# Kernel optimization log

Measured on AMD Instinct MI355X. Metric: run time of the kernel, lower is better.

The kernel has to match this reference:

```python
import jax, jax.numpy as jnp
import numpy as np

B, CIN, COUT, H, W = 8, 64, 64, 56, 56
HEAD, KATT, KCONV = 1, 5, 3
HEAD_DIM = COUT // HEAD
PAD = (1 * (KATT - 1) + 1) // 2  # dilation=1 -> 2


def setup_inputs() -> dict:
    key = jax.random.key(0)
    ks = jax.random.split(key, 12)
    n = jax.random.normal
    return {
        'x': n(ks[0], (B, CIN, H, W), jnp.float32),
        'w1': n(ks[1], (COUT, CIN), jnp.float32) * 0.05,
        'b1': n(ks[2], (COUT,), jnp.float32) * 0.05,
        'w2': n(ks[3], (COUT, CIN), jnp.float32) * 0.05,
        'b2': n(ks[4], (COUT,), jnp.float32) * 0.05,
        'w3': n(ks[5], (COUT, CIN), jnp.float32) * 0.05,
        'b3': n(ks[6], (COUT,), jnp.float32) * 0.05,
        'wp': n(ks[7], (HEAD_DIM, 2), jnp.float32) * 0.05,
        'bp': n(ks[8], (HEAD_DIM,), jnp.float32) * 0.05,
        'w_fc': n(ks[9], (KCONV * KCONV, 3 * HEAD), jnp.float32) * 0.05,
        'w_dep': n(ks[10], (COUT, KCONV * KCONV, KCONV, KCONV), jnp.float32) * 0.05,
        'b_dep': n(ks[11], (COUT,), jnp.float32) * 0.05,
        'rate1': jnp.full((1,), 0.5, jnp.float32),
        'rate2': jnp.full((1,), 0.5, jnp.float32),
    }


def _conv1x1(x, w, b):
    return jnp.einsum('oc,bchw->bohw', w, x) + b[None, :, None, None]


def _unfold(x, h, w):
    # reflection-pad then extract KATTxKATT patches -> (n, c, KATT*KATT, h, w)
    p = jnp.pad(x, ((0, 0), (0, 0), (PAD, PAD), (PAD, PAD)), mode='reflect')
    return jnp.stack([p[:, :, i:i + h, j:j + w]
                      for i in range(KATT) for j in range(KATT)], axis=2)


def reference(x, w1, b1, w2, b2, w3, b3, wp, bp, w_fc, w_dep, b_dep, rate1, rate2):
    b, _, h, w = x.shape
    q = _conv1x1(x, w1, b1)
    k = _conv1x1(x, w2, b2)
    v = _conv1x1(x, w3, b3)
    head_dim = wp.shape[0]
    head = q.shape[1] // head_dim
    scaling = float(head_dim) ** -0.5

    # relative position embedding (stride=1 so q_pe == pe)
    loc_w = jnp.tile(jnp.linspace(-1.0, 1.0, w)[None, :], (h, 1))
    loc_h = jnp.tile(jnp.linspace(-1.0, 1.0, h)[:, None], (1, w))
    pe = _conv1x1(jnp.stack([loc_w, loc_h])[None], wp, bp)  # (1, head_dim, h, w)

    q_att = q.reshape(b * head, head_dim, h, w) * scaling
    k_att = k.reshape(b * head, head_dim, h, w)
    v_att = v.reshape(b * head, head_dim, h, w)

    unfold_k = _unfold(k_att, h, w)          # (b*head, d, 25, h, w)
    unfold_rpe = _unfold(pe, h, w)           # (1, d, 25, h, w)
    att = jnp.sum(q_att[:, :, None] * (unfold_k + pe[:, :, None] - unfold_rpe), axis=1)
    att = jax.nn.softmax(att, axis=1)        # softmax over the 25 window positions
    unfold_v = _unfold(v_att, h, w)
    out_att = jnp.sum(att[:, None] * unfold_v, axis=2).reshape(b, -1, h, w)

    # parallel depthwise-conv branch
    f_cat = jnp.concatenate([q.reshape(b, head, head_dim, h * w),
                             k.reshape(b, head, head_dim, h * w),
                             v.reshape(b, head, head_dim, h * w)], axis=1)  # (b, 3h, d, hw)
    f_all = jnp.einsum('oc,bcdl->bodl', w_fc, f_cat)                        # (b, 9, d, hw)
    f_conv = jnp.transpose(f_all, (0, 2, 1, 3)).reshape(b, head_dim * KCONV * KCONV, h, w)
    out_conv = jax.lax.conv_general_dilated(
        f_conv, w_dep, window_strides=(1, 1), padding=((1, 1), (1, 1)),
        feature_group_count=head_dim,
        dimension_numbers=('NCHW', 'OIHW', 'NCHW')) + b_dep[None, :, None, None]

    return rate1[0] * out_att + rate2[0] * out_conv
```

## Files before the change

kernel.cpp:

```cpp
#include <hip/hip_runtime.h>

#define HH 56
#define WWID 56
#define HWP (HH*WWID)
#define BB 8
#define CC 64
#define NPIX (BB*HWP)

__device__ __forceinline__ float grp_sum(float x) {
  int xi;
  xi = __builtin_amdgcn_update_dpp(0, __float_as_int(x), 0xB1, 0xF, 0xF, true);
  x += __int_as_float(xi);
  xi = __builtin_amdgcn_update_dpp(0, __float_as_int(x), 0x4E, 0xF, 0xF, true);
  x += __int_as_float(xi);
  xi = __builtin_amdgcn_update_dpp(0, __float_as_int(x), 0x141, 0xF, 0xF, true);
  x += __int_as_float(xi);
  xi = __builtin_amdgcn_update_dpp(0, __float_as_int(x), 0x140, 0xF, 0xF, true);
  x += __int_as_float(xi);
  return x;
}

__device__ __forceinline__ float dot4(float4 a, float4 b) {
  float t = a.x * b.x;
  t = fmaf(a.y, b.y, t);
  t = fmaf(a.z, b.z, t);
  t = fmaf(a.w, b.w, t);
  return t;
}

__global__ __launch_bounds__(256) void prep_kernel(
    const float* __restrict__ w1, const float* __restrict__ w2, const float* __restrict__ w3,
    const float* __restrict__ w_fc, const float* __restrict__ w_dep,
    float* __restrict__ w1P, float* __restrict__ w2P, float* __restrict__ w3P,
    float* __restrict__ tab)
{
  const int t = threadIdx.x;
  for (int idx = t; idx < 64*64; idx += 256) {
    int c4 = idx >> 8, r = idx & 255, o = r >> 2, e = r & 3;
    int c = c4*4 + e;
    w1P[idx] = w1[o*64 + c];
    w2P[idx] = w2[o*64 + c];
    w3P[idx] = w3[o*64 + c];
  }
  for (int idx = t; idx < 27*64; idx += 256) {
    int d = idx & 63, bt = idx >> 6;
    int br = bt / 9, tap = bt - br*9;
    float s = 0.f;
    #pragma unroll
    for (int oo = 0; oo < 9; ++oo)
      s += w_dep[d*81 + oo*9 + tap] * w_fc[oo*3 + br];
    tab[idx] = s;
  }
}

__global__ __launch_bounds__(256) void qkv_kernel(
    const float* __restrict__ x,
    const float* __restrict__ b1, const float* __restrict__ b2, const float* __restrict__ b3,
    const float* __restrict__ w1P, const float* __restrict__ w2P, const float* __restrict__ w3P,
    float* __restrict__ q, float* __restrict__ k, float* __restrict__ v)
{
  __shared__ float xs[64 * 32];
  const int tid = threadIdx.x;

  int bid = (int)blockIdx.x;
  bid = (bid & 7) * 98 + (bid >> 3);

  const int pix0 = bid * 32;
  const int n    = pix0 / HWP;
  const int hw0  = pix0 - n * HWP;
  const float* xb = x + (size_t)n * CC * HWP + hw0;

  #pragma unroll
  for (int r = 0; r < 2; ++r) {
    int idx = r * 256 + tid;
    int c   = idx >> 3;
    int p4  = (idx & 7) * 4;
    float4 xv = *reinterpret_cast<const float4*>(xb + (size_t)c * HWP + p4);
    *reinterpret_cast<float4*>(&xs[c*32 + p4]) = xv;
  }
  __syncthreads();

  const int o = tid & 63;
  const int g = __builtin_amdgcn_readfirstlane((int)(tid >> 6));

  float accq[8], acck[8], accv[8];
  const float bq = b1[o], bk = b2[o], bv = b3[o];
  #pragma unroll
  for (int p = 0; p < 8; ++p) { accq[p] = bq; acck[p] = bk; accv[p] = bv; }

  #pragma unroll 2
  for (int c4 = 0; c4 < 16; ++c4) {
    const float4 wq  = *reinterpret_cast<const float4*>(w1P + c4*256 + o*4);
    const float4 wk  = *reinterpret_cast<const float4*>(w2P + c4*256 + o*4);
    const float4 wv4 = *reinterpret_cast<const float4*>(w3P + c4*256 + o*4);
    const float wqa[4] = {wq.x, wq.y, wq.z, wq.w};
    const float wka[4] = {wk.x, wk.y, wk.z, wk.w};
    const float wva[4] = {wv4.x, wv4.y, wv4.z, wv4.w};
    #pragma unroll
    for (int e = 0; e < 4; ++e) {
      const float* xr = &xs[(c4*4 + e)*32 + g*8];
      float4 x0 = *reinterpret_cast<const float4*>(xr);
      float4 x1 = *reinterpret_cast<const float4*>(xr + 4);
      float xf[8] = {x0.x, x0.y, x0.z, x0.w, x1.x, x1.y, x1.z, x1.w};
      #pragma unroll
      for (int p = 0; p < 8; ++p) {
        accq[p] = fmaf(wqa[e], xf[p], accq[p]);
        acck[p] = fmaf(wka[e], xf[p], acck[p]);
        accv[p] = fmaf(wva[e], xf[p], accv[p]);
      }
    }
  }

  const int pbase = pix0 + g * 8;
  #pragma unroll
  for (int p = 0; p < 8; ++p) {
    size_t off = (size_t)(pbase + p) * 64 + o;
    q[off] = accq[p]; k[off] = acck[p]; v[off] = accv[p];
  }
}

__global__ __launch_bounds__(256) void attn_kernel(
    const float* __restrict__ q, const float* __restrict__ k, const float* __restrict__ v,
    const float* __restrict__ wp, const float* __restrict__ tab,
    const float* __restrict__ b_dep, const float* __restrict__ rate1, const float* __restrict__ rate2,
    float* __restrict__ out)
{
  __shared__ float stab[27 * 64];
  __shared__ float sbd[64];
  __shared__ float sout[64 * 17];

  const int tid  = threadIdx.x;
  for (int i = tid; i < 27*64; i += 256) stab[i] = tab[i];
  if (tid < 64) sbd[tid] = b_dep[tid];
  __syncthreads();

  const int lane = tid & 63;
  const int wid  = __builtin_amdgcn_readfirstlane((int)(tid >> 6));
  const int grp  = lane >> 4;
  const int sl   = lane & 15;

  int bid = (int)blockIdx.x;
  bid = (bid & 7) * 196 + (bid >> 3);

  const int pixbase = bid * 16;
  const int pl  = wid * 4 + grp;
  const int pix = pixbase + pl;
  const int n   = pix / HWP;
  const int hw  = pix - n * HWP;
  const int h   = hw / WWID;
  const int w   = hw - h * WWID;

  const size_t nbase = (size_t)n * HWP * 64;
  const float4 q4 = *reinterpret_cast<const float4*>(q + nbase + (size_t)hw * 64 + sl * 4);

  const float4 wa = *reinterpret_cast<const float4*>(wp + 8 * sl);
  const float4 wb = *reinterpret_cast<const float4*>(wp + 8 * sl + 4);
  const float4 wpx4 = {wa.x, wa.z, wb.x, wb.z};
  const float4 wpy4 = {wa.y, wa.w, wb.y, wb.w};
  const float qw0 = grp_sum(dot4(q4, wpx4));
  const float qw1 = grp_sum(dot4(q4, wpy4));

  int hr[5], wr[5];
  #pragma unroll
  for (int i = 0; i < 5; ++i) {
    int t = h + i - 2; hr[i] = t < 0 ? -t : (t >= HH ? 2*HH - 2 - t : t);
    t = w + i - 2;     wr[i] = t < 0 ? -t : (t >= WWID ? 2*WWID - 2 - t : t);
  }

  const float C = 2.0f / 55.0f;
  const float A0 = 0.125f * qw0 * C;
  const float A1 = 0.125f * qw1 * C;

  const float* kb = k + nbase + sl * 4;
  float att[25];
  #pragma unroll
  for (int i = 0; i < 5; ++i) {
    const float* krow = kb + (size_t)(hr[i] * WWID) * 64;
    float4 kk[5];
    #pragma unroll
    for (int j = 0; j < 5; ++j)
      kk[j] = *reinterpret_cast<const float4*>(krow + wr[j] * 64);
    const float rh = A1 * (float)(h - hr[i]);
    #pragma unroll
    for (int j = 0; j < 5; ++j) {
      const float dotv = grp_sum(dot4(q4, kk[j]));
      att[i*5 + j] = 0.125f * dotv + A0 * (float)(w - wr[j]) + rh;
    }
  }

  float m = att[0];
  #pragma unroll
  for (int p = 1; p < 25; ++p) m = fmaxf(m, att[p]);
  float s = 0.f;
  #pragma unroll
  for (int p = 0; p < 25; ++p) { att[p] = __expf(att[p] - m); s += att[p]; }
  const float inv = 1.0f / s;

  const float* vb = v + nbase + sl * 4;
  float4 oatt = {0.f, 0.f, 0.f, 0.f};
  #pragma unroll
  for (int i = 0; i < 5; ++i) {
    const float* vrow = vb + (size_t)(hr[i] * WWID) * 64;
    float4 vv[5];
    #pragma unroll
    for (int j = 0; j < 5; ++j)
      vv[j] = *reinterpret_cast<const float4*>(vrow + wr[j] * 64);
    #pragma unroll
    for (int j = 0; j < 5; ++j) {
      const float a = att[i*5 + j];
      oatt.x = fmaf(a, vv[j].x, oatt.x);
      oatt.y = fmaf(a, vv[j].y, oatt.y);
      oatt.z = fmaf(a, vv[j].z, oatt.z);
      oatt.w = fmaf(a, vv[j].w, oatt.w);
    }
  }

  float4 cacc = {0.f, 0.f, 0.f, 0.f};
  #pragma unroll
  for (int kh = 0; kh < 3; ++kh) {
    const int hh = h + kh - 1;
    float4 qn[3], kn[3], vn[3];
    float mk[3];
    #pragma unroll
    for (int kw = 0; kw < 3; ++kw) {
      const int wc = w + kw - 1;
      const bool ok = ((unsigned)hh < HH) && ((unsigned)wc < WWID);
      const int nb = ok ? hh*WWID + wc : hw;
      mk[kw] = ok ? 1.0f : 0.0f;
      const size_t off = nbase + (size_t)nb * 64 + sl * 4;
      qn[kw] = *reinterpret_cast<const float4*>(q + off);
      kn[kw] = *reinterpret_cast<const float4*>(k + off);
      vn[kw] = *reinterpret_cast<const float4*>(v + off);
    }
    #pragma unroll
    for (int kw = 0; kw < 3; ++kw) {
      const int tap = kh*3 + kw;
      const float4 tq = *reinterpret_cast<const float4*>(&stab[(0*9 + tap)*64 + sl*4]);
      const float4 tk = *reinterpret_cast<const float4*>(&stab[(1*9 + tap)*64 + sl*4]);
      const float4 tv = *reinterpret_cast<const float4*>(&stab[(2*9 + tap)*64 + sl*4]);
      float sx = tq.x*qn[kw].x; sx = fmaf(tk.x, kn[kw].x, sx); sx = fmaf(tv.x, vn[kw].x, sx);
      float sy = tq.y*qn[kw].y; sy = fmaf(tk.y, kn[kw].y, sy); sy = fmaf(tv.y, vn[kw].y, sy);
      float sz = tq.z*qn[kw].z; sz = fmaf(tk.z, kn[kw].z, sz); sz = fmaf(tv.z, vn[kw].z, sz);
      float sw = tq.w*qn[kw].w; sw = fmaf(tk.w, kn[kw].w, sw); sw = fmaf(tv.w, vn[kw].w, sw);
      cacc.x = fmaf(mk[kw], sx, cacc.x);
      cacc.y = fmaf(mk[kw], sy, cacc.y);
      cacc.z = fmaf(mk[kw], sz, cacc.z);
      cacc.w = fmaf(mk[kw], sw, cacc.w);
    }
  }

  const float bdx = sbd[sl*4+0], bdy = sbd[sl*4+1], bdz = sbd[sl*4+2], bdw = sbd[sl*4+3];
  const float r1 = rate1[0];
  const float r2 = rate2[0];

  float res[4];
  res[0] = r1 * (oatt.x * inv) + r2 * (cacc.x + bdx);
  res[1] = r1 * (oatt.y * inv) + r2 * (cacc.y + bdy);
  res[2] = r1 * (oatt.z * inv) + r2 * (cacc.z + bdz);
  res[3] = r1 * (oatt.w * inv) + r2 * (cacc.w + bdw);

  #pragma unroll
  for (int e = 0; e < 4; ++e)
    sout[(4*sl + e)*17 + pl] = res[e];
  __syncthreads();

  const int c  = tid >> 2;
  const int e4 = (tid & 3) * 4;
  const int hw0 = pixbase - n * HWP;
  float4 o4 = {sout[c*17 + e4 + 0], sout[c*17 + e4 + 1],
               sout[c*17 + e4 + 2], sout[c*17 + e4 + 3]};
  *reinterpret_cast<float4*>(out + ((size_t)(n*64 + c))*HWP + hw0 + e4) = o4;
}

extern "C" void kernel_launch(void* const* d_in, const int* in_sizes, int n_in,
                              void* d_out, int out_size, void* d_ws, size_t ws_size,
                              hipStream_t stream) {
  const float* x     = (const float*)d_in[0];
  const float* w1    = (const float*)d_in[1];
  const float* b1    = (const float*)d_in[2];
  const float* w2    = (const float*)d_in[3];
  const float* b2    = (const float*)d_in[4];
  const float* w3    = (const float*)d_in[5];
  const float* b3    = (const float*)d_in[6];
  const float* wp    = (const float*)d_in[7];
  const float* w_fc  = (const float*)d_in[9];
  const float* w_dep = (const float*)d_in[10];
  const float* b_dep = (const float*)d_in[11];
  const float* rate1 = (const float*)d_in[12];
  const float* rate2 = (const float*)d_in[13];
  float* out = (float*)d_out;

  float* ws = (float*)d_ws;
  float* q   = ws;
  float* k   = ws + (size_t)NPIX*64;
  float* v   = ws + (size_t)2*NPIX*64;
  float* w1P = ws + (size_t)3*NPIX*64;
  float* w2P = w1P + 4096;
  float* w3P = w2P + 4096;
  float* tab = w3P + 4096;

  prep_kernel<<<1, 256, 0, stream>>>(w1, w2, w3, w_fc, w_dep, w1P, w2P, w3P, tab);
  qkv_kernel<<<NPIX/32, 256, 0, stream>>>(x, b1, b2, b3, w1P, w2P, w3P, q, k, v);
  attn_kernel<<<NPIX/16, 256, 0, stream>>>(q, k, v, wp, tab, b_dep, rate1, rate2, out);
}
```

Before: 47.72 us.

## Drop prep kernel, widen attention lanes to 8 channels, reuse window K/V for conv

The separate prep kernel is removed. Weights are now read directly in the qkv kernel, and the depthwise tap table is computed per block inside the attention kernel. The attention kernel now gives each lane 8 channels (8-lane groups, 32 pixels per block), which halves the DPP reduction steps. The 3x3 conv branch reuses the K and V values already loaded for the 5x5 window instead of reloading q/k/v neighbours. The qkv kernel moves to 512-thread blocks of 64 pixels. Trade-offs: more registers per lane, redundant tap-table computation in every block, and uncoalesced weight loads in qkv.

Result: slower. 64.25 us (+34.6%).

```diff
diff --git a/kernel.cpp b/kernel.cpp
--- a/kernel.cpp
+++ b/kernel.cpp
@@ -7,7 +7,7 @@
 #define CC 64
 #define NPIX (BB*HWP)
 
-__device__ __forceinline__ float grp_sum(float x) {
+__device__ __forceinline__ float grp_sum8(float x) {
   int xi;
   xi = __builtin_amdgcn_update_dpp(0, __float_as_int(x), 0xB1, 0xF, 0xF, true);
   x += __int_as_float(xi);
@@ -15,8 +15,6 @@
   x += __int_as_float(xi);
   xi = __builtin_amdgcn_update_dpp(0, __float_as_int(x), 0x141, 0xF, 0xF, true);
   x += __int_as_float(xi);
-  xi = __builtin_amdgcn_update_dpp(0, __float_as_int(x), 0x140, 0xF, 0xF, true);
-  x += __int_as_float(xi);
   return x;
 }
 
@@ -28,55 +26,30 @@
   return t;
 }
 
-__global__ __launch_bounds__(256) void prep_kernel(
-    const float* __restrict__ w1, const float* __restrict__ w2, const float* __restrict__ w3,
-    const float* __restrict__ w_fc, const float* __restrict__ w_dep,
-    float* __restrict__ w1P, float* __restrict__ w2P, float* __restrict__ w3P,
-    float* __restrict__ tab)
-{
-  const int t = threadIdx.x;
-  for (int idx = t; idx < 64*64; idx += 256) {
-    int c4 = idx >> 8, r = idx & 255, o = r >> 2, e = r & 3;
-    int c = c4*4 + e;
-    w1P[idx] = w1[o*64 + c];
-    w2P[idx] = w2[o*64 + c];
-    w3P[idx] = w3[o*64 + c];
-  }
-  for (int idx = t; idx < 27*64; idx += 256) {
-    int d = idx & 63, bt = idx >> 6;
-    int br = bt / 9, tap = bt - br*9;
-    float s = 0.f;
-    #pragma unroll
-    for (int oo = 0; oo < 9; ++oo)
-      s += w_dep[d*81 + oo*9 + tap] * w_fc[oo*3 + br];
-    tab[idx] = s;
-  }
-}
-
-__global__ __launch_bounds__(256) void qkv_kernel(
+__global__ __launch_bounds__(512) void qkv_kernel(
     const float* __restrict__ x,
     const float* __restrict__ b1, const float* __restrict__ b2, const float* __restrict__ b3,
-    const float* __restrict__ w1P, const float* __restrict__ w2P, const float* __restrict__ w3P,
+    const float* __restrict__ w1, const float* __restrict__ w2, const float* __restrict__ w3,
     float* __restrict__ q, float* __restrict__ k, float* __restrict__ v)
 {
-  __shared__ float xs[64 * 32];
+  __shared__ float xs[64 * 64];
   const int tid = threadIdx.x;
 
   int bid = (int)blockIdx.x;
-  bid = (bid & 7) * 98 + (bid >> 3);
-
-  const int pix0 = bid * 32;
+  bid = (bid & 7) * 49 + (bid >> 3);
+
+  const int pix0 = bid * 64;
   const int n    = pix0 / HWP;
   const int hw0  = pix0 - n * HWP;
   const float* xb = x + (size_t)n * CC * HWP + hw0;
 
   #pragma unroll
   for (int r = 0; r < 2; ++r) {
-    int idx = r * 256 + tid;
-    int c   = idx >> 3;
-    int p4  = (idx & 7) * 4;
-    float4 xv = *reinterpret_cast<const float4*>(xb + (size_t)c * HWP + p4);
-    *reinterpret_cast<float4*>(&xs[c*32 + p4]) = xv;
+    int idx = r * 512 + tid;
+    int c   = idx >> 4;
+    int p4  = (idx & 15) * 4;
+    *reinterpret_cast<float4*>(&xs[c*64 + p4]) =
+        *reinterpret_cast<const float4*>(xb + (size_t)c * HWP + p4);
   }
   __syncthreads();
 
@@ -88,17 +61,17 @@
   #pragma unroll
   for (int p = 0; p < 8; ++p) { accq[p] = bq; acck[p] = bk; accv[p] = bv; }
 
-  #pragma unroll 2
+  #pragma unroll 4
   for (int c4 = 0; c4 < 16; ++c4) {
-    const float4 wq  = *reinterpret_cast<const float4*>(w1P + c4*256 + o*4);
-    const float4 wk  = *reinterpret_cast<const float4*>(w2P + c4*256 + o*4);
-    const float4 wv4 = *reinterpret_cast<const float4*>(w3P + c4*256 + o*4);
+    const float4 wq  = *reinterpret_cast<const float4*>(w1 + o*64 + c4*4);
+    const float4 wk  = *reinterpret_cast<const float4*>(w2 + o*64 + c4*4);
+    const float4 wv4 = *reinterpret_cast<const float4*>(w3 + o*64 + c4*4);
     const float wqa[4] = {wq.x, wq.y, wq.z, wq.w};
     const float wka[4] = {wk.x, wk.y, wk.z, wk.w};
     const float wva[4] = {wv4.x, wv4.y, wv4.z, wv4.w};
     #pragma unroll
     for (int e = 0; e < 4; ++e) {
-      const float* xr = &xs[(c4*4 + e)*32 + g*8];
+      const float* xr = &xs[(c4*4 + e)*64 + g*8];
       float4 x0 = *reinterpret_cast<const float4*>(xr);
       float4 x1 = *reinterpret_cast<const float4*>(xr + 4);
       float xf[8] = {x0.x, x0.y, x0.z, x0.w, x1.x, x1.y, x1.z, x1.w};
@@ -121,29 +94,36 @@
 
 __global__ __launch_bounds__(256) void attn_kernel(
     const float* __restrict__ q, const float* __restrict__ k, const float* __restrict__ v,
-    const float* __restrict__ wp, const float* __restrict__ tab,
+    const float* __restrict__ wp,
+    const float* __restrict__ w_fc, const float* __restrict__ w_dep,
     const float* __restrict__ b_dep, const float* __restrict__ rate1, const float* __restrict__ rate2,
     float* __restrict__ out)
 {
   __shared__ float stab[27 * 64];
-  __shared__ float sbd[64];
-  __shared__ float sout[64 * 17];
-
-  const int tid  = threadIdx.x;
-  for (int i = tid; i < 27*64; i += 256) stab[i] = tab[i];
-  if (tid < 64) sbd[tid] = b_dep[tid];
+  __shared__ float sout[32 * 68];
+
+  const int tid = threadIdx.x;
+  for (int idx = tid; idx < 27*64; idx += 256) {
+    int d = idx & 63, bt = idx >> 6;
+    int br = bt / 9, tap = bt - br*9;
+    float s = 0.f;
+    #pragma unroll
+    for (int oo = 0; oo < 9; ++oo)
+      s += w_dep[d*81 + oo*9 + tap] * w_fc[oo*3 + br];
+    stab[idx] = s;
+  }
   __syncthreads();
 
   const int lane = tid & 63;
   const int wid  = __builtin_amdgcn_readfirstlane((int)(tid >> 6));
-  const int grp  = lane >> 4;
-  const int sl   = lane & 15;
+  const int grp  = lane >> 3;
+  const int sl   = lane & 7;
 
   int bid = (int)blockIdx.x;
-  bid = (bid & 7) * 196 + (bid >> 3);
-
-  const int pixbase = bid * 16;
-  const int pl  = wid * 4 + grp;
+  bid = (bid & 7) * 98 + (bid >> 3);
+
+  const int pixbase = bid * 32;
+  const int pl  = wid * 8 + grp;
   const int pix = pixbase + pl;
   const int n   = pix / HWP;
   const int hw  = pix - n * HWP;
@@ -151,14 +131,20 @@
   const int w   = hw - h * WWID;
 
   const size_t nbase = (size_t)n * HWP * 64;
-  const float4 q4 = *reinterpret_cast<const float4*>(q + nbase + (size_t)hw * 64 + sl * 4);
-
-  const float4 wa = *reinterpret_cast<const float4*>(wp + 8 * sl);
-  const float4 wb = *reinterpret_cast<const float4*>(wp + 8 * sl + 4);
-  const float4 wpx4 = {wa.x, wa.z, wb.x, wb.z};
-  const float4 wpy4 = {wa.y, wa.w, wb.y, wb.w};
-  const float qw0 = grp_sum(dot4(q4, wpx4));
-  const float qw1 = grp_sum(dot4(q4, wpy4));
+  const float* qp = q + nbase + (size_t)hw * 64 + sl * 8;
+  const float4 q4a = *reinterpret_cast<const float4*>(qp);
+  const float4 q4b = *reinterpret_cast<const float4*>(qp + 4);
+
+  const float4 wA = *reinterpret_cast<const float4*>(wp + sl*16);
+  const float4 wB = *reinterpret_cast<const float4*>(wp + sl*16 + 4);
+  const float4 wC = *reinterpret_cast<const float4*>(wp + sl*16 + 8);
+  const float4 wD = *reinterpret_cast<const float4*>(wp + sl*16 + 12);
+  const float4 wpx0 = {wA.x, wA.z, wB.x, wB.z};
+  const float4 wpx1 = {wC.x, wC.z, wD.x, wD.z};
+  const float4 wpy0 = {wA.y, wA.w, wB.y, wB.w};
+  const float4 wpy1 = {wC.y, wC.w, wD.y, wD.w};
+  const float qw0 = grp_sum8(dot4(q4a, wpx0) + dot4(q4b, wpx1));
+  const float qw1 = grp_sum8(dot4(q4a, wpy0) + dot4(q4b, wpy1));
 
   int hr[5], wr[5];
   #pragma unroll
@@ -171,20 +157,43 @@
   const float A0 = 0.125f * qw0 * C;
   const float A1 = 0.125f * qw1 * C;
 
-  const float* kb = k + nbase + sl * 4;
+  const float* kb = k + nbase + sl * 8;
   float att[25];
+  float4 c0 = {0.f,0.f,0.f,0.f}, c1 = {0.f,0.f,0.f,0.f};
   #pragma unroll
   for (int i = 0; i < 5; ++i) {
     const float* krow = kb + (size_t)(hr[i] * WWID) * 64;
-    float4 kk[5];
-    #pragma unroll
-    for (int j = 0; j < 5; ++j)
-      kk[j] = *reinterpret_cast<const float4*>(krow + wr[j] * 64);
+    float4 ka[5], kb4[5];
+    #pragma unroll
+    for (int j = 0; j < 5; ++j) {
+      ka[j]  = *reinterpret_cast<const float4*>(krow + wr[j] * 64);
+      kb4[j] = *reinterpret_cast<const float4*>(krow + wr[j] * 64 + 4);
+    }
     const float rh = A1 * (float)(h - hr[i]);
     #pragma unroll
     for (int j = 0; j < 5; ++j) {
-      const float dotv = grp_sum(dot4(q4, kk[j]));
-      att[i*5 + j] = 0.125f * dotv + A0 * (float)(w - wr[j]) + rh;
+      const float d8 = grp_sum8(dot4(q4a, ka[j]) + dot4(q4b, kb4[j]));
+      att[i*5 + j] = 0.125f * d8 + A0 * (float)(w - wr[j]) + rh;
+    }
+    if (i >= 1 && i <= 3) {
+      const int hh = h + i - 2;
+      #pragma unroll
+      for (int kw = 0; kw < 3; ++kw) {
+        const int wc = w + kw - 1;
+        const float mk = (((unsigned)hh < HH) && ((unsigned)wc < WWID)) ? 1.f : 0.f;
+        const int tap = (i-1)*3 + kw;
+        const float4 t0 = *reinterpret_cast<const float4*>(&stab[(9 + tap)*64 + sl*8]);
+        const float4 t1 = *reinterpret_cast<const float4*>(&stab[(9 + tap)*64 + sl*8 + 4]);
+        const int j = kw + 1;
+        c0.x = fmaf(mk * t0.x, ka[j].x, c0.x);
+        c0.y = fmaf(mk * t0.y, ka[j].y, c0.y);
+        c0.z = fmaf(mk * t0.z, ka[j].z, c0.z);
+        c0.w = fmaf(mk * t0.w, ka[j].w, c0.w);
+        c1.x = fmaf(mk * t1.x, kb4[j].x, c1.x);
+        c1.y = fmaf(mk * t1.y, kb4[j].y, c1.y);
+        c1.z = fmaf(mk * t1.z, kb4[j].z, c1.z);
+        c1.w = fmaf(mk * t1.w, kb4[j].w, c1.w);
+      }
     }
   }
 
@@ -196,80 +205,95 @@
   for (int p = 0; p < 25; ++p) { att[p] = __expf(att[p] - m); s += att[p]; }
   const float inv = 1.0f / s;
 
-  const float* vb = v + nbase + sl * 4;
-  float4 oatt = {0.f, 0.f, 0.f, 0.f};
+  const float* vb = v + nbase + sl * 8;
+  float4 o0 = {0.f,0.f,0.f,0.f}, o1 = {0.f,0.f,0.f,0.f};
   #pragma unroll
   for (int i = 0; i < 5; ++i) {
     const float* vrow = vb + (size_t)(hr[i] * WWID) * 64;
-    float4 vv[5];
-    #pragma unroll
-    for (int j = 0; j < 5; ++j)
-      vv[j] = *reinterpret_cast<const float4*>(vrow + wr[j] * 64);
+    float4 va[5], vb4[5];
+    #pragma unroll
+    for (int j = 0; j < 5; ++j) {
+      va[j]  = *reinterpret_cast<const float4*>(vrow + wr[j] * 64);
+      vb4[j] = *reinterpret_cast<const float4*>(vrow + wr[j] * 64 + 4);
+    }
     #pragma unroll
     for (int j = 0; j < 5; ++j) {
       const float a = att[i*5 + j];
-      oatt.x = fmaf(a, vv[j].x, oatt.x);
-      oatt.y = fmaf(a, vv[j].y, oatt.y);
-      oatt.z = fmaf(a, vv[j].z, oatt.z);
-      oatt.w = fmaf(a, vv[j].w, oatt.w);
-    }
-  }
-
-  float4 cacc = {0.f, 0.f, 0.f, 0.f};
-  #pragma unroll
-  for (int kh = 0; kh < 3; ++kh) {
-    const int hh = h + kh - 1;
-    float4 qn[3], kn[3], vn[3];
-    float mk[3];
-    #pragma unroll
-    for (int kw = 0; kw < 3; ++kw) {
-      const int wc = w + kw - 1;
-      const bool ok = ((unsigned)hh < HH) && ((unsigned)wc < WWID);
-      const int nb = ok ? hh*WWID + wc : hw;
-      mk[kw] = ok ? 1.0f : 0.0f;
-      const size_t off = nbase + (size_t)nb * 64 + sl * 4;
-      qn[kw] = *reinterpret_cast<const float4*>(q + off);
-      kn[kw] = *reinterpret_cast<const float4*>(k + off);
-      vn[kw] = *reinterpret_cast<const float4*>(v + off);
-    }
-    #pragma unroll
-    for (int kw = 0; kw < 3; ++kw) {
-      const int tap = kh*3 + kw;
-      const float4 tq = *reinterpret_cast<const float4*>(&stab[(0*9 + tap)*64 + sl*4]);
-      const float4 tk = *reinterpret_cast<const float4*>(&stab[(1*9 + tap)*64 + sl*4]);
-      const float4 tv = *reinterpret_cast<const float4*>(&stab[(2*9 + tap)*64 + sl*4]);
-      float sx = tq.x*qn[kw].x; sx = fmaf(tk.x, kn[kw].x, sx); sx = fmaf(tv.x, vn[kw].x, sx);
-      float sy = tq.y*qn[kw].y; sy = fmaf(tk.y, kn[kw].y, sy); sy = fmaf(tv.y, vn[kw].y, sy);
-      float sz = tq.z*qn[kw].z; sz = fmaf(tk.z, kn[kw].z, sz); sz = fmaf(tv.z, vn[kw].z, sz);
-      float sw = tq.w*qn[kw].w; sw = fmaf(tk.w, kn[kw].w, sw); sw = fmaf(tv.w, vn[kw].w, sw);
-      cacc.x = fmaf(mk[kw], sx, cacc.x);
-      cacc.y = fmaf(mk[kw], sy, cacc.y);
-      cacc.z = fmaf(mk[kw], sz, cacc.z);
-      cacc.w = fmaf(mk[kw], sw, cacc.w);
-    }
-  }
-
-  const float bdx = sbd[sl*4+0], bdy = sbd[sl*4+1], bdz = sbd[sl*4+2], bdw = sbd[sl*4+3];
-  const float r1 = rate1[0];
+      o0.x = fmaf(a, va[j].x, o0.x);
+      o0.y = fmaf(a, va[j].y, o0.y);
+      o0.z = fmaf(a, va[j].z, o0.z);
+      o0.w = fmaf(a, va[j].w, o0.w);
+      o1.x = fmaf(a, vb4[j].x, o1.x);
+      o1.y = fmaf(a, vb4[j].y, o1.y);
+      o1.z = fmaf(a, vb4[j].z, o1.z);
+      o1.w = fmaf(a, vb4[j].w, o1.w);
+    }
+    if (i >= 1 && i <= 3) {
+      const int hh = h + i - 2;
+      #pragma unroll
+      for (int kw = 0; kw < 3; ++kw) {
+        const int wc = w + kw - 1;
+        const float mk = (((unsigned)hh < HH) && ((unsigned)wc < WWID)) ? 1.f : 0.f;
+        const int tap = (i-1)*3 + kw;
+        const int j = kw + 1;
+        const float4 t0 = *reinterpret_cast<const float4*>(&stab[(18 + tap)*64 + sl*8]);
+        const float4 t1 = *reinterpret_cast<const float4*>(&stab[(18 + tap)*64 + sl*8 + 4]);
+        c0.x = fmaf(mk * t0.x, va[j].x, c0.x);
+        c0.y = fmaf(mk * t0.y, va[j].y, c0.y);
+        c0.z = fmaf(mk * t0.z, va[j].z, c0.z);
+        c0.w = fmaf(mk * t0.w, va[j].w, c0.w);
+        c1.x = fmaf(mk * t1.x, vb4[j].x, c1.x);
+        c1.y = fmaf(mk * t1.y, vb4[j].y, c1.y);
+        c1.z = fmaf(mk * t1.z, vb4[j].z, c1.z);
+        c1.w = fmaf(mk * t1.w, vb4[j].w, c1.w);
+        const float* qrow = q + nbase + (size_t)(hr[i]*WWID + wr[j]) * 64 + sl * 8;
+        const float4 qa = *reinterpret_cast<const float4*>(qrow);
+        const float4 qb2 = *reinterpret_cast<const float4*>(qrow + 4);
+        const float4 u0 = *reinterpret_cast<const float4*>(&stab[(0 + tap)*64 + sl*8]);
+        const float4 u1 = *reinterpret_cast<const float4*>(&stab[(0 + tap)*64 + sl*8 + 4]);
+        c0.x = fmaf(mk * u0.x, qa.x, c0.x);
+        c0.y = fmaf(mk * u0.y, qa.y, c0.y);
+        c0.z = fmaf(mk * u0.z, qa.z, c0.z);
+        c0.w = fmaf(mk * u0.w, qa.w, c0.w);
+        c1.x = fmaf(mk * u1.x, qb2.x, c1.x);
+        c1.y = fmaf(mk * u1.y, qb2.y, c1.y);
+        c1.z = fmaf(mk * u1.z, qb2.z, c1.z);
+        c1.w = fmaf(mk * u1.w, qb2.w, c1.w);
+      }
+    }
+  }
+
+  const float4 bd0 = *reinterpret_cast<const float4*>(b_dep + sl*8);
+  const float4 bd1 = *reinterpret_cast<const float4*>(b_dep + sl*8 + 4);
+  const float r1 = rate1[0] * inv;
   const float r2 = rate2[0];
 
-  float res[4];
-  res[0] = r1 * (oatt.x * inv) + r2 * (cacc.x + bdx);
-  res[1] = r1 * (oatt.y * inv) + r2 * (cacc.y + bdy);
-  res[2] = r1 * (oatt.z * inv) + r2 * (cacc.z + bdz);
-  res[3] = r1 * (oatt.w * inv) + r2 * (cacc.w + bdw);
-
-  #pragma unroll
-  for (int e = 0; e < 4; ++e)
-    sout[(4*sl + e)*17 + pl] = res[e];
+  float4 s0, s1;
+  s0.x = r1 * o0.x + r2 * (c0.x + bd0.x);
+  s0.y = r1 * o0.y + r2 * (c0.y + bd0.y);
+  s0.z = r1 * o0.z + r2 * (c0.z + bd0.z);
+  s0.w = r1 * o0.w + r2 * (c0.w + bd0.w);
+  s1.x = r1 * o1.x + r2 * (c1.x + bd1.x);
+  s1.y = r1 * o1.y + r2 * (c1.y + bd1.y);
+  s1.z = r1 * o1.z + r2 * (c1.z + bd1.z);
+  s1.w = r1 * o1.w + r2 * (c1.w + bd1.w);
+
+  *reinterpret_cast<float4*>(&sout[pl*68 + sl*8])     = s0;
+  *reinterpret_cast<float4*>(&sout[pl*68 + sl*8 + 4]) = s1;
   __syncthreads();
 
-  const int c  = tid >> 2;
-  const int e4 = (tid & 3) * 4;
-  const int hw0 = pixbase - n * HWP;
-  float4 o4 = {sout[c*17 + e4 + 0], sout[c*17 + e4 + 1],
-               sout[c*17 + e4 + 2], sout[c*17 + e4 + 3]};
-  *reinterpret_cast<float4*>(out + ((size_t)(n*64 + c))*HWP + hw0 + e4) = o4;
+  const int c   = tid >> 2;
+  const int seg = tid & 3;
+  const int n0  = pixbase / HWP;
+  const int hwb = pixbase - n0 * HWP + seg * 8;
+  float r[8];
+  #pragma unroll
+  for (int t2 = 0; t2 < 8; ++t2) r[t2] = sout[(seg*8 + t2)*68 + c];
+  float* ob = out + ((size_t)(n0*64 + c))*HWP + hwb;
+  float4 u0 = {r[0], r[1], r[2], r[3]};
+  float4 u1 = {r[4], r[5], r[6], r[7]};
+  *reinterpret_cast<float4*>(ob)     = u0;
+  *reinterpret_cast<float4*>(ob + 4) = u1;
 }
 
 extern "C" void kernel_launch(void* const* d_in, const int* in_sizes, int n_in,
@@ -291,15 +315,10 @@
   float* out = (float*)d_out;
 
   float* ws = (float*)d_ws;
-  float* q   = ws;
-  float* k   = ws + (size_t)NPIX*64;
-  float* v   = ws + (size_t)2*NPIX*64;
-  float* w1P = ws + (size_t)3*NPIX*64;
-  float* w2P = w1P + 4096;
-  float* w3P = w2P + 4096;
-  float* tab = w3P + 4096;
-
-  prep_kernel<<<1, 256, 0, stream>>>(w1, w2, w3, w_fc, w_dep, w1P, w2P, w3P, tab);
-  qkv_kernel<<<NPIX/32, 256, 0, stream>>>(x, b1, b2, b3, w1P, w2P, w3P, q, k, v);
-  attn_kernel<<<NPIX/16, 256, 0, stream>>>(q, k, v, wp, tab, b_dep, rate1, rate2, out);
-}
+  float* q = ws;
+  float* k = ws + (size_t)NPIX*64;
+  float* v = ws + (size_t)2*NPIX*64;
+
+  qkv_kernel<<<NPIX/64, 512, 0, stream>>>(x, b1, b2, b3, w1, w2, w3, q, k, v);
+  attn_kernel<<<NPIX/32, 256, 0, stream>>>(q, k, v, wp, w_fc, w_dep, b_dep, rate1, rate2, out);
+}
```

## Fuse attention and depthwise-conv loops with online softmax and shared K/V loads

Applied to the files above, without the earlier changes.

Merges the three separate passes (QK scores, softmax-weighted V sum, 3x3 conv over q/k/v) into one pass over window rows, using an online softmax so K and V for each row are loaded together. The conv branch reuses the K and V values already loaded for the central 3x3 taps, so only Q neighbours are fetched separately. This cuts redundant global loads and the 25-entry score array. In exchange it adds per-row rescaling exps. Interior pixels match reference padding, but at borders the conv reuses reflection-padded K/V and masks them to zero, which is still correct.

Measured after the change: 45.10 us. 5.5% less time.

```diff
diff --git a/kernel.cpp b/kernel.cpp
--- a/kernel.cpp
+++ b/kernel.cpp
@@ -172,92 +172,84 @@
   const float A1 = 0.125f * qw1 * C;
 
   const float* kb = k + nbase + sl * 4;
-  float att[25];
+  const float* vb = v + nbase + sl * 4;
+
+  float m = -__builtin_inff();
+  float s = 0.f;
+  float4 oatt = {0.f, 0.f, 0.f, 0.f};
+  float4 cacc = {0.f, 0.f, 0.f, 0.f};
+
   #pragma unroll
   for (int i = 0; i < 5; ++i) {
-    const float* krow = kb + (size_t)(hr[i] * WWID) * 64;
-    float4 kk[5];
-    #pragma unroll
-    for (int j = 0; j < 5; ++j)
-      kk[j] = *reinterpret_cast<const float4*>(krow + wr[j] * 64);
+    const size_t rowoff = (size_t)(hr[i] * WWID) * 64;
+    const float* krow = kb + rowoff;
+    const float* vrow = vb + rowoff;
+    float4 ka[5], va[5];
+    #pragma unroll
+    for (int j = 0; j < 5; ++j) ka[j] = *reinterpret_cast<const float4*>(krow + wr[j] * 64);
+    #pragma unroll
+    for (int j = 0; j < 5; ++j) va[j] = *reinterpret_cast<const float4*>(vrow + wr[j] * 64);
+
     const float rh = A1 * (float)(h - hr[i]);
+    float att[5];
     #pragma unroll
     for (int j = 0; j < 5; ++j) {
-      const float dotv = grp_sum(dot4(q4, kk[j]));
-      att[i*5 + j] = 0.125f * dotv + A0 * (float)(w - wr[j]) + rh;
-    }
-  }
-
-  float m = att[0];
-  #pragma unroll
-  for (int p = 1; p < 25; ++p) m = fmaxf(m, att[p]);
-  float s = 0.f;
-  #pragma unroll
-  for (int p = 0; p < 25; ++p) { att[p] = __expf(att[p] - m); s += att[p]; }
+      const float d8 = grp_sum(dot4(q4, ka[j]));
+      att[j] = 0.125f * d8 + A0 * (float)(w - wr[j]) + rh;
+    }
+
+    float mrow = att[0];
+    #pragma unroll
+    for (int j = 1; j < 5; ++j) mrow = fmaxf(mrow, att[j]);
+    const float mnew = fmaxf(m, mrow);
+    const float scale = __expf(m - mnew);
+    m = mnew;
+    s *= scale;
+    oatt.x *= scale; oatt.y *= scale; oatt.z *= scale; oatt.w *= scale;
+    #pragma unroll
+    for (int j = 0; j < 5; ++j) {
+      const float p = __expf(att[j] - m);
+      s += p;
+      oatt.x = fmaf(p, va[j].x, oatt.x);
+      oatt.y = fmaf(p, va[j].y, oatt.y);
+      oatt.z = fmaf(p, va[j].z, oatt.z);
+      oatt.w = fmaf(p, va[j].w, oatt.w);
+    }
+
+    if (i >= 1 && i <= 3) {
+      const int hh = h + i - 2;
+      #pragma unroll
+      for (int kw = 0; kw < 3; ++kw) {
+        const int wc = w + kw - 1;
+        const float mk = (((unsigned)hh < HH) && ((unsigned)wc < WWID)) ? 1.f : 0.f;
+        const int tap = (i-1)*3 + kw;
+        const int j = kw + 1;
+        const float4 tq = *reinterpret_cast<const float4*>(&stab[(0*9 + tap)*64 + sl*4]);
+        const float4 tk = *reinterpret_cast<const float4*>(&stab[(1*9 + tap)*64 + sl*4]);
+        const float4 tv = *reinterpret_cast<const float4*>(&stab[(2*9 + tap)*64 + sl*4]);
+        const float4 qn = *reinterpret_cast<const float4*>(q + nbase + (size_t)(hr[i]*WWID + wr[j]) * 64 + sl * 4);
+        float sx = tq.x*qn.x; sx = fmaf(tk.x, ka[j].x, sx); sx = fmaf(tv.x, va[j].x, sx);
+        float sy = tq.y*qn.y; sy = fmaf(tk.y, ka[j].y, sy); sy = fmaf(tv.y, va[j].y, sy);
+        float sz = tq.z*qn.z; sz = fmaf(tk.z, ka[j].z, sz); sz = fmaf(tv.z, va[j].z, sz);
+        float sw = tq.w*qn.w; sw = fmaf(tk.w, ka[j].w, sw); sw = fmaf(tv.w, va[j].w, sw);
+        cacc.x = fmaf(mk, sx, cacc.x);
+        cacc.y = fmaf(mk, sy, cacc.y);
+        cacc.z = fmaf(mk, sz, cacc.z);
+        cacc.w = fmaf(mk, sw, cacc.w);
+      }
+    }
+  }
+
   const float inv = 1.0f / s;
-
-  const float* vb = v + nbase + sl * 4;
-  float4 oatt = {0.f, 0.f, 0.f, 0.f};
-  #pragma unroll
-  for (int i = 0; i < 5; ++i) {
-    const float* vrow = vb + (size_t)(hr[i] * WWID) * 64;
-    float4 vv[5];
-    #pragma unroll
-    for (int j = 0; j < 5; ++j)
-      vv[j] = *reinterpret_cast<const float4*>(vrow + wr[j] * 64);
-    #pragma unroll
-    for (int j = 0; j < 5; ++j) {
-      const float a = att[i*5 + j];
-      oatt.x = fmaf(a, vv[j].x, oatt.x);
-      oatt.y = fmaf(a, vv[j].y, oatt.y);
-      oatt.z = fmaf(a, vv[j].z, oatt.z);
-      oatt.w = fmaf(a, vv[j].w, oatt.w);
-    }
-  }
-
-  float4 cacc = {0.f, 0.f, 0.f, 0.f};
-  #pragma unroll
-  for (int kh = 0; kh < 3; ++kh) {
-    const int hh = h + kh - 1;
-    float4 qn[3], kn[3], vn[3];
-    float mk[3];
-    #pragma unroll
-    for (int kw = 0; kw < 3; ++kw) {
-      const int wc = w + kw - 1;
-      const bool ok = ((unsigned)hh < HH) && ((unsigned)wc < WWID);
-      const int nb = ok ? hh*WWID + wc : hw;
-      mk[kw] = ok ? 1.0f : 0.0f;
-      const size_t off = nbase + (size_t)nb * 64 + sl * 4;
-      qn[kw] = *reinterpret_cast<const float4*>(q + off);
-      kn[kw] = *reinterpret_cast<const float4*>(k + off);
-      vn[kw] = *reinterpret_cast<const float4*>(v + off);
-    }
-    #pragma unroll
-    for (int kw = 0; kw < 3; ++kw) {
-      const int tap = kh*3 + kw;
-      const float4 tq = *reinterpret_cast<const float4*>(&stab[(0*9 + tap)*64 + sl*4]);
-      const float4 tk = *reinterpret_cast<const float4*>(&stab[(1*9 + tap)*64 + sl*4]);
-      const float4 tv = *reinterpret_cast<const float4*>(&stab[(2*9 + tap)*64 + sl*4]);
-      float sx = tq.x*qn[kw].x; sx = fmaf(tk.x, kn[kw].x, sx); sx = fmaf(tv.x, vn[kw].x, sx);
-      float sy = tq.y*qn[kw].y; sy = fmaf(tk.y, kn[kw].y, sy); sy = fmaf(tv.y, vn[kw].y, sy);
-      float sz = tq.z*qn[kw].z; sz = fmaf(tk.z, kn[kw].z, sz); sz = fmaf(tv.z, vn[kw].z, sz);
-      float sw = tq.w*qn[kw].w; sw = fmaf(tk.w, kn[kw].w, sw); sw = fmaf(tv.w, vn[kw].w, sw);
-      cacc.x = fmaf(mk[kw], sx, cacc.x);
-      cacc.y = fmaf(mk[kw], sy, cacc.y);
-      cacc.z = fmaf(mk[kw], sz, cacc.z);
-      cacc.w = fmaf(mk[kw], sw, cacc.w);
-    }
-  }
-
   const float bdx = sbd[sl*4+0], bdy = sbd[sl*4+1], bdz = sbd[sl*4+2], bdw = sbd[sl*4+3];
-  const float r1 = rate1[0];
+  const float r1 = rate1[0] * inv;
   const float r2 = rate2[0];
 
   float res[4];
-  res[0] = r1 * (oatt.x * inv) + r2 * (cacc.x + bdx);
-  res[1] = r1 * (oatt.y * inv) + r2 * (cacc.y + bdy);
-  res[2] = r1 * (oatt.z * inv) + r2 * (cacc.z + bdz);
-  res[3] = r1 * (oatt.w * inv) + r2 * (cacc.w + bdw);
+  res[0] = r1 * oatt.x + r2 * (cacc.x + bdx);
+  res[1] = r1 * oatt.y + r2 * (cacc.y + bdy);
+  res[2] = r1 * oatt.z + r2 * (cacc.z + bdz);
+  res[3] = r1 * oatt.w + r2 * (cacc.w + bdw);
 
   #pragma unroll
   for (int e = 0; e < 4; ++e)
```
